# Kernel optimization log

Hardware: AMD Instinct MI355X
Metric: run time of the kernel (lower is better)

Reference implementation:

```python
import jax, jax.numpy as jnp
import numpy as np

B, N, C, D = 16, 2048, 256, 256


def setup_inputs() -> dict:
    key = jax.random.key(0)
    ks = jax.random.split(key, 8)
    x = jax.random.normal(ks[0], (B, N, C), dtype=jnp.float32)
    valid_len = jax.random.randint(ks[1], (B,), 0, N)
    # nn.Linear params: weight [out, in], bias [out]
    s = 1.0 / np.sqrt(C)
    Wq = jax.random.uniform(ks[2], (D, C), dtype=jnp.float32, minval=-s, maxval=s)
    bq = jax.random.uniform(ks[3], (D,), dtype=jnp.float32, minval=-s, maxval=s)
    Wk = jax.random.uniform(ks[4], (D, C), dtype=jnp.float32, minval=-s, maxval=s)
    bk = jax.random.uniform(ks[5], (D,), dtype=jnp.float32, minval=-s, maxval=s)
    Wv = jax.random.uniform(ks[6], (D, C), dtype=jnp.float32, minval=-s, maxval=s)
    bv = jax.random.uniform(ks[7], (D,), dtype=jnp.float32, minval=-s, maxval=s)
    return {"x": x, "valid_len": valid_len, "Wq": Wq, "bq": bq,
            "Wk": Wk, "bk": bk, "Wv": Wv, "bv": bv}


def reference(x, valid_len, Wq, bq, Wk, bk, Wv, bv):
    # QKV projections (nn.Linear: x @ W^T + b)
    q = jnp.einsum('bnc,dc->bnd', x, Wq) + bq
    k = jnp.einsum('bnc,dc->bnd', x, Wk) + bk
    v = jnp.einsum('bnc,dc->bnd', x, Wv) + bv
    # scores [B, N, N] = q @ k^T (no scaling: scale_factor_d unused in forward)
    scores = jnp.einsum('bnd,bmd->bnm', q, k)
    # key-side valid-length mask: arange(N) < valid_len[b], broadcast over queries
    mask = jnp.arange(N)[None, :] < valid_len[:, None]          # [B, N]
    scores = jnp.where(mask[:, None, :], scores, jnp.float32(-1000000.0))
    attn = jax.nn.softmax(scores, axis=-1)
    return jnp.einsum('bnm,bmd->bnd', attn, v)
```

## Files before the change

### kernel.cpp

```cpp
#include <hip/hip_runtime.h>
#include <hip/hip_bf16.h>
#include <stdint.h>

typedef __attribute__((ext_vector_type(8))) _Float16 half8;
typedef __attribute__((ext_vector_type(4))) _Float16 half4;
typedef __attribute__((ext_vector_type(2))) __fp16 fp16x2;
typedef __attribute__((ext_vector_type(4))) float f32x4;
typedef __attribute__((ext_vector_type(16))) float f32x16;
typedef __attribute__((ext_vector_type(4))) float float4v;

#define DEVI static __device__ __forceinline__

constexpr int Bb = 16, Nn = 2048, Cc = 256, Dd = 256;

DEVI unsigned short f2h_bits(float f) {
  _Float16 h = (_Float16)f;
  union { _Float16 h; unsigned short u; } c;
  c.h = h;
  return c.u;
}

DEVI void gl_lds16(const void* gsrc, void* ldst) {
  __builtin_amdgcn_global_load_lds(
      (const __attribute__((address_space(1))) unsigned int*)gsrc,
      (__attribute__((address_space(3))) unsigned int*)ldst, 16, 0, 0);
}

DEVI f32x4 mfma16h(half8 a, half8 b, f32x4 c) {
  return __builtin_amdgcn_mfma_f32_16x16x32_f16(a, b, c, 0, 0, 0);
}
DEVI f32x16 mfma32h(half8 a, half8 b, f32x16 c) {
  return __builtin_amdgcn_mfma_f32_32x32x16_f16(a, b, c, 0, 0, 0);
}

DEVI unsigned int pkrtz(float a, float b) {
  union { fp16x2 h; unsigned int u; } c;
  c.h = __builtin_amdgcn_cvt_pkrtz(a, b);
  return c.u;
}

__global__ void k_split(const float* __restrict__ x, const float* __restrict__ wq,
                        const float* __restrict__ wk, const float* __restrict__ wv,
                        _Float16* __restrict__ xh, _Float16* __restrict__ wh) {
  int i = blockIdx.x * 256 + threadIdx.x;
  if (i < 2097152) {
    float4v v = reinterpret_cast<const float4v*>(x)[i];
    half4 h;
#pragma unroll
    for (int j = 0; j < 4; ++j) h[j] = (_Float16)v[j];
    reinterpret_cast<half4*>(xh)[i] = h;
  } else {
    int ii = i - 2097152;
    int mat = ii >> 16;
    int rem = ii & 65535;
    const float* w = (mat == 0) ? wq : ((mat == 1) ? wk : wv);
    wh[(size_t)mat * 65536 + rem] = (_Float16)w[rem];
  }
}

__global__ __launch_bounds__(256, 2) void k_qkv(
    const _Float16* __restrict__ xh, const _Float16* __restrict__ wh,
    const float* __restrict__ bq, const float* __restrict__ bk, const float* __restrict__ bv,
    _Float16* __restrict__ qout, _Float16* __restrict__ kout, _Float16* __restrict__ vt) {
  __shared__ __align__(16) unsigned short smem[17408];

  const int tid = threadIdx.x;
  const int m0 = blockIdx.x * 128;
  const int n0 = blockIdx.y * 128;
  const int mat = blockIdx.z;
  const _Float16* wmat = wh + (size_t)mat * 65536;
  const int wave = tid >> 6, lane = tid & 63;
  const int wr = wave >> 1, wc = wave & 1;
  const int l15 = lane & 15, lq = lane >> 4;

  f32x4 zero4 = {0.f, 0.f, 0.f, 0.f};
  f32x4 acc[4][4];
#pragma unroll
  for (int a = 0; a < 4; ++a)
#pragma unroll
    for (int b2 = 0; b2 < 4; ++b2) acc[a][b2] = zero4;

  char* As = (char*)smem;
  char* Bs = (char*)smem + 16384;

  for (int kc = 0; kc < 4; ++kc) {
#pragma unroll
    for (int i = 0; i < 4; ++i) {
      int p = i * 4096 + tid * 16;
      int row = p >> 7;
      int src_in_row = (p & 127) ^ ((row & 7) << 4);
      const char* g = (const char*)(xh + (size_t)(m0 + row) * Cc + kc * 64) + src_in_row;
      gl_lds16(g, As + p);
    }
#pragma unroll
    for (int i = 0; i < 4; ++i) {
      int p = i * 4096 + tid * 16;
      int row = p >> 7;
      int src_in_row = (p & 127) ^ ((row & 7) << 4);
      const char* g = (const char*)(wmat + (size_t)(n0 + row) * Cc + kc * 64) + src_in_row;
      gl_lds16(g, Bs + p);
    }
    __syncthreads();
#pragma unroll
    for (int ks = 0; ks < 2; ++ks) {
      half8 af[4], bfr[4];
#pragma unroll
      for (int mf = 0; mf < 4; ++mf) {
        int row = wr * 64 + mf * 16 + l15;
        int byte = (row * 128 + ks * 64 + lq * 16) ^ ((row & 7) << 4);
        af[mf] = *(const half8*)(As + byte);
      }
#pragma unroll
      for (int nf = 0; nf < 4; ++nf) {
        int row = wc * 64 + nf * 16 + l15;
        int byte = (row * 128 + ks * 64 + lq * 16) ^ ((row & 7) << 4);
        bfr[nf] = *(const half8*)(Bs + byte);
      }
#pragma unroll
      for (int mf = 0; mf < 4; ++mf)
#pragma unroll
        for (int nf = 0; nf < 4; ++nf) acc[mf][nf] = mfma16h(af[mf], bfr[nf], acc[mf][nf]);
    }
    __syncthreads();
  }

  const float* bias = (mat == 0) ? bq : ((mat == 1) ? bk : bv);
  if (mat < 2) {
    _Float16* oo = (mat == 0) ? qout : kout;
#pragma unroll
    for (int nf = 0; nf < 4; ++nf) {
      int col = n0 + wc * 64 + nf * 16 + l15;
      float bval = bias[col];
#pragma unroll
      for (int mf = 0; mf < 4; ++mf) {
        int grow = m0 + wr * 64 + mf * 16 + lq * 4;
#pragma unroll
        for (int r = 0; r < 4; ++r)
          oo[(size_t)(grow + r) * Dd + col] = (_Float16)(acc[mf][nf][r] + bval);
      }
    }
  } else {
    __syncthreads();
#pragma unroll
    for (int nf = 0; nf < 4; ++nf) {
      int dl = wc * 64 + nf * 16 + l15;
      float bval = bias[n0 + dl];
#pragma unroll
      for (int mf = 0; mf < 4; ++mf) {
        int nl = wr * 64 + mf * 16 + lq * 4;
#pragma unroll
        for (int r = 0; r < 4; ++r) smem[dl * 136 + nl + r] = f2h_bits(acc[mf][nf][r] + bval);
      }
    }
    __syncthreads();
    const int bbat = m0 >> 11, tok0 = m0 & 2047;
#pragma unroll
    for (int pss = 0; pss < 8; ++pss) {
      int idx = pss * 256 + tid;
      int dl = idx >> 4;
      int cu = idx & 15;
      half8 vval = *(const half8*)((const char*)smem + dl * 272 + cu * 16);
      size_t off = ((size_t)bbat * Dd + n0 + dl) * Nn + tok0 + cu * 8;
      *(half8*)(vt + off) = vval;
    }
  }
}

__global__ __launch_bounds__(256, 2) void k_attn_p(
    const _Float16* __restrict__ qg, const _Float16* __restrict__ kin,
    const _Float16* __restrict__ vt, const int* __restrict__ vlen,
    _Float16* __restrict__ Op, float* __restrict__ ml) {
  __shared__ __align__(16) char SMEM[66048];
  char* const Kb = SMEM;
  char* const Vb = SMEM + 32768;
  unsigned int* const PL = (unsigned int*)SMEM;
  float* const mex = (float*)(SMEM + 65536);

  const int tid = threadIdx.x;
  const int wave = tid >> 6, lane = tid & 63;
  const int l31 = lane & 31, h = lane >> 5;
  const int wq = wave >> 1, wk = wave & 1;
  const int id = blockIdx.x;
  const int g = id & 7;
  const int b = g + 8 * (id >> 9);
  const int q0 = ((id >> 4) & 31) * 64;
  const int kh = (id >> 3) & 1;
  const int kst = kh * 1024;
  const int L = vlen[b];
  const bool uni = (L == 0);
  const int Lk = uni ? Nn : L;
  const int avail = Lk - kst;
  const int nt = (avail > 0) ? ((avail + 63) >> 6 < 16 ? (avail + 63) >> 6 : 16) : 0;
  const size_t prow = (size_t)(b * 2 + kh) * Nn + q0;

  if (nt == 0) {
    if (tid < 64) {
      ml[(prow + tid) * 2 + 0] = -1e30f;
      ml[(prow + tid) * 2 + 1] = 0.f;
    }
    return;
  }

  const char* kbase = (const char*)(kin + (size_t)b * Nn * Dd);
  const char* vbase = (const char*)(vt + (size_t)b * Dd * Nn);
  const char* qbase = (const char*)(qg + ((size_t)b * Nn + q0) * Dd);

#pragma unroll
  for (int i = 0; i < 8; ++i) {
    int p = i * 4096 + tid * 16;
    int row = p >> 9;
    int sl = ((p & 511) >> 4) ^ (row & 31);
    gl_lds16(qbase + (size_t)row * 512 + (sl << 4), Kb + p);
  }
  asm volatile("s_waitcnt vmcnt(0)" ::: "memory");
  asm volatile("s_barrier" ::: "memory");
  half8 qreg[16];
  {
    const int row = wq * 32 + l31;
#pragma unroll
    for (int kt = 0; kt < 16; ++kt) {
      int byte = row * 512 + (((kt * 2 + h) ^ (row & 31)) << 4);
      qreg[kt] = *(const half8*)(Kb + byte);
    }
  }
  asm volatile("s_waitcnt lgkmcnt(0)" ::: "memory");
  asm volatile("s_barrier" ::: "memory");

  f32x16 acc[4];
#pragma unroll
  for (int dg = 0; dg < 4; ++dg)
#pragma unroll
    for (int r = 0; r < 16; ++r) acc[dg][r] = 0.f;
  float m = -__builtin_inff();
  float lsum = 0.f;

  for (int t = 0; t < nt; ++t) {
    const int k0 = kst + t * 64;
#pragma unroll
    for (int i = 0; i < 8; ++i) {
      int p = i * 4096 + tid * 16;
      int row = p >> 9;
      int sl = ((p & 511) >> 4) ^ (row & 31);
      gl_lds16(kbase + (size_t)(k0 + row) * 512 + (sl << 4), Kb + p);
    }
#pragma unroll
    for (int i = 0; i < 8; ++i) {
      int p = i * 4096 + tid * 16;
      int r = p >> 9;
      int sl = ((p & 511) >> 4) ^ (r & 31);
      int cl = sl << 4;
      int d = r * 4 + (cl >> 7);
      int kbyte = cl & 127;
      gl_lds16(vbase + (size_t)d * (Nn * 2) + (size_t)k0 * 2 + kbyte, Vb + p);
    }
    asm volatile("s_waitcnt vmcnt(0)" ::: "memory");
    asm volatile("s_barrier" ::: "memory");

    f32x16 st;
#pragma unroll
    for (int r = 0; r < 16; ++r) st[r] = 0.f;
    if (!uni) {
      const int key = wk * 32 + l31;
      __builtin_amdgcn_s_setprio(1);
#pragma unroll
      for (int kt = 0; kt < 16; ++kt) {
        int byte = key * 512 + (((kt * 2 + h) ^ l31) << 4);
        half8 kf = *(const half8*)(Kb + byte);
        st = mfma32h(kf, qreg[kt], st);
      }
      __builtin_amdgcn_s_setprio(0);
      if (k0 + 64 > L) {
#pragma unroll
        for (int r = 0; r < 16; ++r) {
          int keyg = k0 + wk * 32 + (r & 3) + 8 * (r >> 2) + 4 * h;
          if (keyg >= L) st[r] = -1e6f;
        }
      }
    }

    float pm = st[0];
#pragma unroll
    for (int r = 1; r < 16; ++r) pm = fmaxf(pm, st[r]);
    pm = fmaxf(pm, __shfl_xor(pm, 32));
    if (lane < 32) mex[wave * 32 + lane] = pm;
    asm volatile("s_waitcnt lgkmcnt(0)\ns_barrier" ::: "memory");
    float pmo = mex[(wave ^ 1) * 32 + l31];
    float mnew = fmaxf(m, fmaxf(pm, pmo));
    float scale = __expf(m - mnew);
    m = mnew;
    float psum = 0.f;
#pragma unroll
    for (int r = 0; r < 16; ++r) {
      float p_ = __expf(st[r] - mnew);
      st[r] = p_;
      psum += p_;
    }
    lsum = lsum * scale + psum;

#pragma unroll
    for (int i = 0; i < 8; ++i) {
      unsigned int pk = pkrtz(st[2 * i], st[2 * i + 1]);
      int kp = wk * 16 + 4 * (i >> 1) + (i & 1) + 2 * h;
      PL[wq * 1024 + kp * 32 + l31] = pk;
    }
    asm volatile("s_waitcnt lgkmcnt(0)\ns_barrier" ::: "memory");

    union { unsigned int u[4]; half8 v; } pf0, pf1, pf2, pf3;
#pragma unroll
    for (int w = 0; w < 4; ++w) {
      pf0.u[w] = PL[wq * 1024 + (0 * 8 + h * 4 + w) * 32 + l31];
      pf1.u[w] = PL[wq * 1024 + (1 * 8 + h * 4 + w) * 32 + l31];
      pf2.u[w] = PL[wq * 1024 + (2 * 8 + h * 4 + w) * 32 + l31];
      pf3.u[w] = PL[wq * 1024 + (3 * 8 + h * 4 + w) * 32 + l31];
    }

#pragma unroll
    for (int dg = 0; dg < 4; ++dg)
#pragma unroll
      for (int r = 0; r < 16; ++r) acc[dg][r] *= scale;

    __builtin_amdgcn_s_setprio(1);
#pragma unroll
    for (int dg = 0; dg < 4; ++dg) {
      int r = wk * 32 + dg * 8 + (l31 >> 2);
#pragma unroll
      for (int ks = 0; ks < 4; ++ks) {
        int slot = (l31 & 3) * 8 + ks * 2 + h;
        half8 vf = *(const half8*)(Vb + r * 512 + ((slot ^ (r & 31)) << 4));
        acc[dg] = mfma32h(vf, ks == 0 ? pf0.v : (ks == 1 ? pf1.v : (ks == 2 ? pf2.v : pf3.v)),
                          acc[dg]);
      }
    }
    __builtin_amdgcn_s_setprio(0);

    asm volatile("s_barrier" ::: "memory");
  }

  lsum += __shfl_xor(lsum, 32);
  if (lane < 32) mex[wave * 32 + lane] = lsum;
  asm volatile("s_waitcnt lgkmcnt(0)\ns_barrier" ::: "memory");
  float ltot = lsum + mex[(wave ^ 1) * 32 + l31];
  float linv = 1.f / ltot;

  if (h == 0 && wk == 0) {
    size_t qq = prow + wq * 32 + l31;
    ml[qq * 2 + 0] = m;
    ml[qq * 2 + 1] = ltot;
  }

  _Float16* T = (_Float16*)SMEM;
  {
    const int ql = wq * 32 + l31;
#pragma unroll
    for (int dg = 0; dg < 4; ++dg)
#pragma unroll
      for (int r = 0; r < 16; ++r) {
        int d = wk * 128 + dg * 32 + (r & 3) + 8 * (r >> 2) + 4 * h;
        T[ql * 264 + d] = (_Float16)(acc[dg][r] * linv);
      }
  }
  asm volatile("s_waitcnt lgkmcnt(0)\ns_barrier" ::: "memory");

  {
    const int rb = tid >> 6;
    const int c4 = (tid & 63) * 4;
#pragma unroll
    for (int i = 0; i < 16; ++i) {
      int row = rb + i * 4;
      half4 v = *(const half4*)(T + row * 264 + c4);
      *(half4*)(Op + (prow + row) * Dd + c4) = v;
    }
  }
}

__global__ __launch_bounds__(256) void k_comb(const _Float16* __restrict__ Op,
                                              const float* __restrict__ ml,
                                              float* __restrict__ out) {
  int rid = blockIdx.x * 4 + (threadIdx.x >> 6);
  int lane = threadIdx.x & 63;
  int b = rid >> 11, q = rid & 2047;
  size_t i0 = (size_t)(b * 2 + 0) * Nn + q;
  size_t i1 = (size_t)(b * 2 + 1) * Nn + q;
  float m0 = ml[i0 * 2], l0 = ml[i0 * 2 + 1];
  float m1 = ml[i1 * 2], l1 = ml[i1 * 2 + 1];
  float M = fmaxf(m0, m1);
  float c0 = (l0 > 0.f) ? __expf(m0 - M) * l0 : 0.f;
  float c1 = (l1 > 0.f) ? __expf(m1 - M) * l1 : 0.f;
  float inv = 1.f / (c0 + c1);
  c0 *= inv;
  c1 *= inv;
  float4v o = {0.f, 0.f, 0.f, 0.f};
  {
    half4 o0 = *(const half4*)(Op + i0 * 256 + lane * 4);
#pragma unroll
    for (int j = 0; j < 4; ++j) o[j] = c0 * (float)o0[j];
  }
  if (c1 > 0.f) {
    half4 o1 = *(const half4*)(Op + i1 * 256 + lane * 4);
#pragma unroll
    for (int j = 0; j < 4; ++j) o[j] += c1 * (float)o1[j];
  }
  *(float4v*)(out + ((size_t)b * Nn + q) * 256 + lane * 4) = o;
}

__global__ __launch_bounds__(512, 2) void k_attn(
    const _Float16* __restrict__ qg, const _Float16* __restrict__ kin,
    const _Float16* __restrict__ vt, const int* __restrict__ vlen,
    float* __restrict__ out) {
  __shared__ __align__(16) char SMEM[149504];
  char* const KVb = SMEM;
  unsigned int* const PL = (unsigned int*)(SMEM + 131072);
  float* const mex = (float*)(SMEM + 147456);
  float* const lex = (float*)(SMEM + 148480);

  const int tid = threadIdx.x;
  const int wave = tid >> 6, lane = tid & 63;
  const int l31 = lane & 31, h = lane >> 5;
  const int wq = wave >> 1, wk = wave & 1;
  const int id = blockIdx.x;
  const int g = id & 7;
  const int j = id >> 3;
  const int b = g + 8 * (j >> 4);
  const int q0 = (j & 15) * 128;
  const int L = vlen[b];
  const bool uni = (L == 0);
  const int Lk = uni ? Nn : L;
  const int nt = (Lk + 63) >> 6;

  const char* kbase = (const char*)(kin + (size_t)b * Nn * Dd);
  const char* vbase = (const char*)(vt + (size_t)b * Dd * Nn);
  const char* qbase = (const char*)(qg + ((size_t)b * Nn + q0) * Dd);

  auto STAGE = [&](int buf, int t) {
    char* dst = KVb + buf * 65536;
    const int k0 = t * 64;
#pragma unroll
    for (int i = 0; i < 4; ++i) {
      int p = i * 8192 + tid * 16;
      int row = p >> 9;
      int sl = ((p & 511) >> 4) ^ (row & 31);
      gl_lds16(kbase + (size_t)(k0 + row) * 512 + (sl << 4), dst + p);
    }
#pragma unroll
    for (int i = 0; i < 4; ++i) {
      int p = i * 8192 + tid * 16;
      int r = p >> 9;
      int sl = ((p & 511) >> 4) ^ (r & 31);
      int cl = sl << 4;
      int d = r * 4 + (cl >> 7);
      int kbyte = cl & 127;
      gl_lds16(vbase + (size_t)d * (Nn * 2) + (size_t)k0 * 2 + kbyte, dst + 32768 + p);
    }
  };

  STAGE(0, 0);
#pragma unroll
  for (int i = 0; i < 8; ++i) {
    int p = i * 8192 + tid * 16;
    int row = p >> 9;
    int sl = ((p & 511) >> 4) ^ (row & 31);
    gl_lds16(qbase + (size_t)row * 512 + (sl << 4), KVb + 65536 + p);
  }
  asm volatile("s_waitcnt vmcnt(0)" ::: "memory");
  asm volatile("s_barrier" ::: "memory");

  half8 qreg[16];
  {
    const int row = wq * 32 + l31;
#pragma unroll
    for (int kt = 0; kt < 16; ++kt) {
      int byte = row * 512 + (((kt * 2 + h) ^ (row & 31)) << 4);
      qreg[kt] = *(const half8*)(KVb + 65536 + byte);
    }
  }
  asm volatile("s_waitcnt lgkmcnt(0)" ::: "memory");
  asm volatile("s_barrier" ::: "memory");

  f32x16 acc[4];
#pragma unroll
  for (int dg = 0; dg < 4; ++dg)
#pragma unroll
    for (int r = 0; r < 16; ++r) acc[dg][r] = 0.f;
  float m = -__builtin_inff();
  float lsum = 0.f;

  for (int t = 0; t < nt; ++t) {
    const int cur = t & 1;
    if (t + 1 < nt) {
      STAGE(cur ^ 1, t + 1);
      asm volatile("s_waitcnt vmcnt(8)" ::: "memory");
    } else {
      asm volatile("s_waitcnt vmcnt(0)" ::: "memory");
    }
    asm volatile("s_barrier" ::: "memory");

    const char* Ks = KVb + cur * 65536;
    const char* Vs = Ks + 32768;
    const int k0 = t * 64;

    f32x16 st;
#pragma unroll
    for (int r = 0; r < 16; ++r) st[r] = 0.f;
    if (!uni) {
      const int key = wk * 32 + l31;
      __builtin_amdgcn_s_setprio(1);
#pragma unroll
      for (int kt = 0; kt < 16; ++kt) {
        int byte = key * 512 + (((kt * 2 + h) ^ l31) << 4);
        half8 kf = *(const half8*)(Ks + byte);
        st = mfma32h(kf, qreg[kt], st);
      }
      __builtin_amdgcn_s_setprio(0);
      if (k0 + 64 > L) {
#pragma unroll
        for (int r = 0; r < 16; ++r) {
          int keyg = k0 + wk * 32 + (r & 3) + 8 * (r >> 2) + 4 * h;
          if (keyg >= L) st[r] = -1e6f;
        }
      }
    }

    float pm = st[0];
#pragma unroll
    for (int r = 1; r < 16; ++r) pm = fmaxf(pm, st[r]);
    pm = fmaxf(pm, __shfl_xor(pm, 32));
    if (lane < 32) mex[wave * 32 + lane] = pm;
    asm volatile("s_waitcnt lgkmcnt(0)\ns_barrier" ::: "memory");
    float pmo = mex[(wave ^ 1) * 32 + l31];
    float mnew = fmaxf(m, fmaxf(pm, pmo));
    float scale = __expf(m - mnew);
    m = mnew;
    float psum = 0.f;
#pragma unroll
    for (int r = 0; r < 16; ++r) {
      float p_ = __expf(st[r] - mnew);
      st[r] = p_;
      psum += p_;
    }
    lsum = lsum * scale + psum;

#pragma unroll
    for (int i = 0; i < 8; ++i) {
      unsigned int pk = pkrtz(st[2 * i], st[2 * i + 1]);
      int kp = wk * 16 + 4 * (i >> 1) + (i & 1) + 2 * h;
      PL[wq * 1024 + kp * 32 + l31] = pk;
    }
    asm volatile("s_waitcnt lgkmcnt(0)\ns_barrier" ::: "memory");

    union { unsigned int u[4]; half8 v; } pf0, pf1, pf2, pf3;
#pragma unroll
    for (int w = 0; w < 4; ++w) {
      pf0.u[w] = PL[wq * 1024 + (0 * 8 + h * 4 + w) * 32 + l31];
      pf1.u[w] = PL[wq * 1024 + (1 * 8 + h * 4 + w) * 32 + l31];
      pf2.u[w] = PL[wq * 1024 + (2 * 8 + h * 4 + w) * 32 + l31];
      pf3.u[w] = PL[wq * 1024 + (3 * 8 + h * 4 + w) * 32 + l31];
    }

#pragma unroll
    for (int dg = 0; dg < 4; ++dg)
#pragma unroll
      for (int r = 0; r < 16; ++r) acc[dg][r] *= scale;

    __builtin_amdgcn_s_setprio(1);
#pragma unroll
    for (int dg = 0; dg < 4; ++dg) {
      int r = wk * 32 + dg * 8 + (l31 >> 2);
#pragma unroll
      for (int ks = 0; ks < 4; ++ks) {
        int slot = (l31 & 3) * 8 + ks * 2 + h;
        half8 vf = *(const half8*)(Vs + r * 512 + ((slot ^ (r & 31)) << 4));
        acc[dg] = mfma32h(vf, ks == 0 ? pf0.v : (ks == 1 ? pf1.v : (ks == 2 ? pf2.v : pf3.v)),
                          acc[dg]);
      }
    }
    __builtin_amdgcn_s_setprio(0);

    asm volatile("s_barrier" ::: "memory");
  }

  lsum += __shfl_xor(lsum, 32);
  if (lane < 32) lex[wave * 32 + lane] = lsum;
  asm volatile("s_waitcnt lgkmcnt(0)\ns_barrier" ::: "memory");
  float linv = 1.f / (lsum + lex[(wave ^ 1) * 32 + l31]);

  float* T = (float*)SMEM;
  {
    const int ql = wq * 32 + l31;
#pragma unroll
    for (int dg = 0; dg < 4; ++dg)
#pragma unroll
      for (int r = 0; r < 16; ++r) {
        int d = wk * 128 + dg * 32 + (r & 3) + 8 * (r >> 2) + 4 * h;
        T[ql * 260 + d] = acc[dg][r] * linv;
      }
  }
  asm volatile("s_waitcnt lgkmcnt(0)\ns_barrier" ::: "memory");

  {
    const int rb = tid >> 6;
    const int c4 = (tid & 63) * 4;
#pragma unroll
    for (int i = 0; i < 16; ++i) {
      int row = rb + i * 8;
      float4v v = *(const float4v*)(T + row * 260 + c4);
      *(float4v*)(out + ((size_t)b * Nn + q0 + row) * Dd + c4) = v;
    }
  }
}

extern "C" void kernel_launch(void* const* d_in, const int* in_sizes, int n_in,
                              void* d_out, int out_size, void* d_ws, size_t ws_size,
                              hipStream_t stream) {
  const float* x = (const float*)d_in[0];
  const int* vlen = (const int*)d_in[1];
  const float* Wq = (const float*)d_in[2];
  const float* bq = (const float*)d_in[3];
  const float* Wk = (const float*)d_in[4];
  const float* bk = (const float*)d_in[5];
  const float* Wv = (const float*)d_in[6];
  const float* bv = (const float*)d_in[7];
  float* out = (float*)d_out;
  char* ws = (char*)d_ws;

  _Float16* qh = (_Float16*)(ws);
  _Float16* kk = (_Float16*)(ws + 16777216);
  _Float16* vt = (_Float16*)(ws + 33554432);
  _Float16* wh = (_Float16*)(ws + 50331648);
  _Float16* Op = (_Float16*)(ws + 51380224);
  float* ml = (float*)(ws + 84934656);
  _Float16* xh = (_Float16*)d_out;

  k_split<<<8960, 256, 0, stream>>>(x, Wq, Wk, Wv, xh, wh);
  k_qkv<<<dim3(256, 2, 3), 256, 0, stream>>>(xh, wh, bq, bk, bv, qh, kk, vt);
  if (ws_size >= 85458944ull) {
    k_attn_p<<<1024, 256, 0, stream>>>(qh, kk, vt, vlen, Op, ml);
    k_comb<<<8192, 256, 0, stream>>>(Op, ml, out);
  } else {
    k_attn<<<256, 512, 0, stream>>>(qh, kk, vt, vlen, out);
  }
}
```

Before: 129.5 us.

## Sort attention work items by cost and pair them in persistent double-buffered blocks

A new tiny kernel computes the number of key tiles for each (batch, 128-query tile, key half) item and sorts the items by descending cost. The attention kernel becomes a 256-block, 512-thread persistent kernel in which each block processes the heaviest remaining item paired with the lightest, to even out load across CUs when valid lengths vary. It also double-buffers the K/V tile loads so global-to-LDS copies overlap the MFMA work, and k_comb now skips loading a partial whose weight is zero. The costs are an extra kernel launch, larger LDS use that allows only one block per CU, and a longer dependency chain inside each block.

```diff
diff --git a/kernel.cpp b/kernel.cpp
--- a/kernel.cpp
+++ b/kernel.cpp
@@ -166,210 +166,250 @@
   }
 }
 
-__global__ __launch_bounds__(256, 2) void k_attn_p(
+__global__ void k_order(const int* __restrict__ vlen, int* __restrict__ order) {
+  __shared__ int nts[512];
+  int t = threadIdx.x;
+  int b = t >> 5, kh = t & 1;
+  int L = vlen[b];
+  int Lk = (L == 0) ? Nn : L;
+  int avail = Lk - kh * 1024;
+  int nt = (avail > 0) ? ((avail + 63) >> 6) : 0;
+  nt = nt > 16 ? 16 : nt;
+  nts[t] = nt;
+  __syncthreads();
+  int rank = 0;
+  for (int j = 0; j < 512; ++j) {
+    int nj = nts[j];
+    if (nj > nt || (nj == nt && j < t)) ++rank;
+  }
+  order[rank] = t;
+}
+
+__global__ __launch_bounds__(512, 2) void k_attn_f(
     const _Float16* __restrict__ qg, const _Float16* __restrict__ kin,
     const _Float16* __restrict__ vt, const int* __restrict__ vlen,
-    _Float16* __restrict__ Op, float* __restrict__ ml) {
-  __shared__ __align__(16) char SMEM[66048];
-  char* const Kb = SMEM;
-  char* const Vb = SMEM + 32768;
-  unsigned int* const PL = (unsigned int*)SMEM;
-  float* const mex = (float*)(SMEM + 65536);
+    const int* __restrict__ order, _Float16* __restrict__ Op,
+    float* __restrict__ ml) {
+  __shared__ __align__(16) char SMEM[149504];
+  char* const KVb = SMEM;
+  unsigned int* const PL = (unsigned int*)(SMEM + 131072);
+  float* const mex = (float*)(SMEM + 147456);
+  float* const lex = (float*)(SMEM + 148480);
 
   const int tid = threadIdx.x;
   const int wave = tid >> 6, lane = tid & 63;
   const int l31 = lane & 31, h = lane >> 5;
   const int wq = wave >> 1, wk = wave & 1;
-  const int id = blockIdx.x;
-  const int g = id & 7;
-  const int b = g + 8 * (id >> 9);
-  const int q0 = ((id >> 4) & 31) * 64;
-  const int kh = (id >> 3) & 1;
-  const int kst = kh * 1024;
-  const int L = vlen[b];
-  const bool uni = (L == 0);
-  const int Lk = uni ? Nn : L;
-  const int avail = Lk - kst;
-  const int nt = (avail > 0) ? ((avail + 63) >> 6 < 16 ? (avail + 63) >> 6 : 16) : 0;
-  const size_t prow = (size_t)(b * 2 + kh) * Nn + q0;
-
-  if (nt == 0) {
-    if (tid < 64) {
-      ml[(prow + tid) * 2 + 0] = -1e30f;
-      ml[(prow + tid) * 2 + 1] = 0.f;
-    }
-    return;
-  }
-
-  const char* kbase = (const char*)(kin + (size_t)b * Nn * Dd);
-  const char* vbase = (const char*)(vt + (size_t)b * Dd * Nn);
-  const char* qbase = (const char*)(qg + ((size_t)b * Nn + q0) * Dd);
-
-#pragma unroll
-  for (int i = 0; i < 8; ++i) {
-    int p = i * 4096 + tid * 16;
-    int row = p >> 9;
-    int sl = ((p & 511) >> 4) ^ (row & 31);
-    gl_lds16(qbase + (size_t)row * 512 + (sl << 4), Kb + p);
-  }
-  asm volatile("s_waitcnt vmcnt(0)" ::: "memory");
-  asm volatile("s_barrier" ::: "memory");
-  half8 qreg[16];
-  {
-    const int row = wq * 32 + l31;
-#pragma unroll
-    for (int kt = 0; kt < 16; ++kt) {
-      int byte = row * 512 + (((kt * 2 + h) ^ (row & 31)) << 4);
-      qreg[kt] = *(const half8*)(Kb + byte);
-    }
-  }
-  asm volatile("s_waitcnt lgkmcnt(0)" ::: "memory");
-  asm volatile("s_barrier" ::: "memory");
-
-  f32x16 acc[4];
-#pragma unroll
-  for (int dg = 0; dg < 4; ++dg)
-#pragma unroll
-    for (int r = 0; r < 16; ++r) acc[dg][r] = 0.f;
-  float m = -__builtin_inff();
-  float lsum = 0.f;
-
-  for (int t = 0; t < nt; ++t) {
-    const int k0 = kst + t * 64;
+
+  for (int s = 0; s < 2; ++s) {
+    const int item = order[s == 0 ? blockIdx.x : (511 - blockIdx.x)];
+    const int b = item >> 5;
+    const int q0 = ((item >> 1) & 15) * 128;
+    const int kh = item & 1;
+    const int kst = kh * 1024;
+    const int L = vlen[b];
+    const bool uni = (L == 0);
+    const int Lk = uni ? Nn : L;
+    const int avail = Lk - kst;
+    int nt = (avail > 0) ? ((avail + 63) >> 6) : 0;
+    nt = nt > 16 ? 16 : nt;
+    const size_t prow = (size_t)(b * 2 + kh) * Nn + q0;
+
+    if (nt == 0) {
+      if (tid < 128) {
+        ml[(prow + tid) * 2 + 0] = -1e30f;
+        ml[(prow + tid) * 2 + 1] = 0.f;
+      }
+      continue;
+    }
+
+    const char* kbase = (const char*)(kin + (size_t)b * Nn * Dd);
+    const char* vbase = (const char*)(vt + (size_t)b * Dd * Nn);
+    const char* qbase = (const char*)(qg + ((size_t)b * Nn + q0) * Dd);
+
+    auto STAGE = [&](int buf, int t) {
+      char* dst = KVb + buf * 65536;
+      const int k0 = kst + t * 64;
+#pragma unroll
+      for (int i = 0; i < 4; ++i) {
+        int p = i * 8192 + tid * 16;
+        int row = p >> 9;
+        int sl = ((p & 511) >> 4) ^ (row & 31);
+        gl_lds16(kbase + (size_t)(k0 + row) * 512 + (sl << 4), dst + p);
+      }
+#pragma unroll
+      for (int i = 0; i < 4; ++i) {
+        int p = i * 8192 + tid * 16;
+        int r = p >> 9;
+        int sl = ((p & 511) >> 4) ^ (r & 31);
+        int cl = sl << 4;
+        int d = r * 4 + (cl >> 7);
+        int kbyte = cl & 127;
+        gl_lds16(vbase + (size_t)d * (Nn * 2) + (size_t)k0 * 2 + kbyte, dst + 32768 + p);
+      }
+    };
+
+    STAGE(0, 0);
 #pragma unroll
     for (int i = 0; i < 8; ++i) {
-      int p = i * 4096 + tid * 16;
+      int p = i * 8192 + tid * 16;
       int row = p >> 9;
       int sl = ((p & 511) >> 4) ^ (row & 31);
-      gl_lds16(kbase + (size_t)(k0 + row) * 512 + (sl << 4), Kb + p);
-    }
-#pragma unroll
-    for (int i = 0; i < 8; ++i) {
-      int p = i * 4096 + tid * 16;
-      int r = p >> 9;
-      int sl = ((p & 511) >> 4) ^ (r & 31);
-      int cl = sl << 4;
-      int d = r * 4 + (cl >> 7);
-      int kbyte = cl & 127;
-      gl_lds16(vbase + (size_t)d * (Nn * 2) + (size_t)k0 * 2 + kbyte, Vb + p);
+      gl_lds16(qbase + (size_t)row * 512 + (sl << 4), KVb + 65536 + p);
     }
     asm volatile("s_waitcnt vmcnt(0)" ::: "memory");
     asm volatile("s_barrier" ::: "memory");
 
-    f32x16 st;
-#pragma unroll
-    for (int r = 0; r < 16; ++r) st[r] = 0.f;
-    if (!uni) {
-      const int key = wk * 32 + l31;
+    half8 qreg[16];
+    {
+      const int row = wq * 32 + l31;
+#pragma unroll
+      for (int kt = 0; kt < 16; ++kt) {
+        int byte = row * 512 + (((kt * 2 + h) ^ (row & 31)) << 4);
+        qreg[kt] = *(const half8*)(KVb + 65536 + byte);
+      }
+    }
+    asm volatile("s_waitcnt lgkmcnt(0)" ::: "memory");
+    asm volatile("s_barrier" ::: "memory");
+
+    f32x16 acc[4];
+#pragma unroll
+    for (int dg = 0; dg < 4; ++dg)
+#pragma unroll
+      for (int r = 0; r < 16; ++r) acc[dg][r] = 0.f;
+    float m = -__builtin_inff();
+    float lsum = 0.f;
+
+    for (int t = 0; t < nt; ++t) {
+      const int cur = t & 1;
+      if (t + 1 < nt) {
+        STAGE(cur ^ 1, t + 1);
+        asm volatile("s_waitcnt vmcnt(8)" ::: "memory");
+      } else {
+        asm volatile("s_waitcnt vmcnt(0)" ::: "memory");
+      }
+      asm volatile("s_barrier" ::: "memory");
+
+      const char* Ks = KVb + cur * 65536;
+      const char* Vs = Ks + 32768;
+      const int k0 = kst + t * 64;
+
+      f32x16 st;
+#pragma unroll
+      for (int r = 0; r < 16; ++r) st[r] = 0.f;
+      if (!uni) {
+        const int key = wk * 32 + l31;
+        __builtin_amdgcn_s_setprio(1);
+#pragma unroll
+        for (int kt = 0; kt < 16; ++kt) {
+          int byte = key * 512 + (((kt * 2 + h) ^ l31) << 4);
+          half8 kf = *(const half8*)(Ks + byte);
+          st = mfma32h(kf, qreg[kt], st);
+        }
+        __builtin_amdgcn_s_setprio(0);
+        if (k0 + 64 > L) {
+#pragma unroll
+          for (int r = 0; r < 16; ++r) {
+            int keyg = k0 + wk * 32 + (r & 3) + 8 * (r >> 2) + 4 * h;
+            if (keyg >= L) st[r] = -1e6f;
+          }
+        }
+      }
+
+      float pm = st[0];
+#pragma unroll
+      for (int r = 1; r < 16; ++r) pm = fmaxf(pm, st[r]);
+      pm = fmaxf(pm, __shfl_xor(pm, 32));
+      if (lane < 32) mex[wave * 32 + lane] = pm;
+      asm volatile("s_waitcnt lgkmcnt(0)\ns_barrier" ::: "memory");
+      float pmo = mex[(wave ^ 1) * 32 + l31];
+      float mnew = fmaxf(m, fmaxf(pm, pmo));
+      float scale = __expf(m - mnew);
+      m = mnew;
+      float psum = 0.f;
+#pragma unroll
+      for (int r = 0; r < 16; ++r) {
+        float p_ = __expf(st[r] - mnew);
+        st[r] = p_;
+        psum += p_;
+      }
+      lsum = lsum * scale + psum;
+
+#pragma unroll
+      for (int i = 0; i < 8; ++i) {
+        unsigned int pk = pkrtz(st[2 * i], st[2 * i + 1]);
+        int kp = wk * 16 + 4 * (i >> 1) + (i & 1) + 2 * h;
+        PL[wq * 1024 + kp * 32 + l31] = pk;
+      }
+      asm volatile("s_waitcnt lgkmcnt(0)\ns_barrier" ::: "memory");
+
+      union { unsigned int u[4]; half8 v; } pf0, pf1, pf2, pf3;
+#pragma unroll
+      for (int w = 0; w < 4; ++w) {
+        pf0.u[w] = PL[wq * 1024 + (0 * 8 + h * 4 + w) * 32 + l31];
+        pf1.u[w] = PL[wq * 1024 + (1 * 8 + h * 4 + w) * 32 + l31];
+        pf2.u[w] = PL[wq * 1024 + (2 * 8 + h * 4 + w) * 32 + l31];
+        pf3.u[w] = PL[wq * 1024 + (3 * 8 + h * 4 + w) * 32 + l31];
+      }
+
+#pragma unroll
+      for (int dg = 0; dg < 4; ++dg)
+#pragma unroll
+        for (int r = 0; r < 16; ++r) acc[dg][r] *= scale;
+
       __builtin_amdgcn_s_setprio(1);
 #pragma unroll
-      for (int kt = 0; kt < 16; ++kt) {
-        int byte = key * 512 + (((kt * 2 + h) ^ l31) << 4);
-        half8 kf = *(const half8*)(Kb + byte);
-        st = mfma32h(kf, qreg[kt], st);
+      for (int dg = 0; dg < 4; ++dg) {
+        int r = wk * 32 + dg * 8 + (l31 >> 2);
+#pragma unroll
+        for (int ks = 0; ks < 4; ++ks) {
+          int slot = (l31 & 3) * 8 + ks * 2 + h;
+          half8 vf = *(const half8*)(Vs + r * 512 + ((slot ^ (r & 31)) << 4));
+          acc[dg] = mfma32h(vf, ks == 0 ? pf0.v : (ks == 1 ? pf1.v : (ks == 2 ? pf2.v : pf3.v)),
+                            acc[dg]);
+        }
       }
       __builtin_amdgcn_s_setprio(0);
-      if (k0 + 64 > L) {
+
+      asm volatile("s_barrier" ::: "memory");
+    }
+
+    lsum += __shfl_xor(lsum, 32);
+    if (lane < 32) lex[wave * 32 + lane] = lsum;
+    asm volatile("s_waitcnt lgkmcnt(0)\ns_barrier" ::: "memory");
+    float ltot = lsum + lex[(wave ^ 1) * 32 + l31];
+    float linv = 1.f / ltot;
+
+    if (h == 0 && wk == 0) {
+      size_t qq = prow + wq * 32 + l31;
+      ml[qq * 2 + 0] = m;
+      ml[qq * 2 + 1] = ltot;
+    }
+
+    _Float16* T = (_Float16*)SMEM;
+    {
+      const int ql = wq * 32 + l31;
+#pragma unroll
+      for (int dg = 0; dg < 4; ++dg)
 #pragma unroll
         for (int r = 0; r < 16; ++r) {
-          int keyg = k0 + wk * 32 + (r & 3) + 8 * (r >> 2) + 4 * h;
-          if (keyg >= L) st[r] = -1e6f;
+          int d = wk * 128 + dg * 32 + (r & 3) + 8 * (r >> 2) + 4 * h;
+          T[ql * 264 + d] = (_Float16)(acc[dg][r] * linv);
         }
-      }
-    }
-
-    float pm = st[0];
-#pragma unroll
-    for (int r = 1; r < 16; ++r) pm = fmaxf(pm, st[r]);
-    pm = fmaxf(pm, __shfl_xor(pm, 32));
-    if (lane < 32) mex[wave * 32 + lane] = pm;
+    }
     asm volatile("s_waitcnt lgkmcnt(0)\ns_barrier" ::: "memory");
-    float pmo = mex[(wave ^ 1) * 32 + l31];
-    float mnew = fmaxf(m, fmaxf(pm, pmo));
-    float scale = __expf(m - mnew);
-    m = mnew;
-    float psum = 0.f;
-#pragma unroll
-    for (int r = 0; r < 16; ++r) {
-      float p_ = __expf(st[r] - mnew);
-      st[r] = p_;
-      psum += p_;
-    }
-    lsum = lsum * scale + psum;
-
-#pragma unroll
-    for (int i = 0; i < 8; ++i) {
-      unsigned int pk = pkrtz(st[2 * i], st[2 * i + 1]);
-      int kp = wk * 16 + 4 * (i >> 1) + (i & 1) + 2 * h;
-      PL[wq * 1024 + kp * 32 + l31] = pk;
+
+    {
+      const int rb = tid >> 6;
+      const int c4 = (tid & 63) * 4;
+#pragma unroll
+      for (int i = 0; i < 16; ++i) {
+        int row = rb + i * 8;
+        half4 v = *(const half4*)(T + row * 264 + c4);
+        *(half4*)(Op + (prow + row) * Dd + c4) = v;
+      }
     }
     asm volatile("s_waitcnt lgkmcnt(0)\ns_barrier" ::: "memory");
-
-    union { unsigned int u[4]; half8 v; } pf0, pf1, pf2, pf3;
-#pragma unroll
-    for (int w = 0; w < 4; ++w) {
-      pf0.u[w] = PL[wq * 1024 + (0 * 8 + h * 4 + w) * 32 + l31];
-      pf1.u[w] = PL[wq * 1024 + (1 * 8 + h * 4 + w) * 32 + l31];
-      pf2.u[w] = PL[wq * 1024 + (2 * 8 + h * 4 + w) * 32 + l31];
-      pf3.u[w] = PL[wq * 1024 + (3 * 8 + h * 4 + w) * 32 + l31];
-    }
-
-#pragma unroll
-    for (int dg = 0; dg < 4; ++dg)
-#pragma unroll
-      for (int r = 0; r < 16; ++r) acc[dg][r] *= scale;
-
-    __builtin_amdgcn_s_setprio(1);
-#pragma unroll
-    for (int dg = 0; dg < 4; ++dg) {
-      int r = wk * 32 + dg * 8 + (l31 >> 2);
-#pragma unroll
-      for (int ks = 0; ks < 4; ++ks) {
-        int slot = (l31 & 3) * 8 + ks * 2 + h;
-        half8 vf = *(const half8*)(Vb + r * 512 + ((slot ^ (r & 31)) << 4));
-        acc[dg] = mfma32h(vf, ks == 0 ? pf0.v : (ks == 1 ? pf1.v : (ks == 2 ? pf2.v : pf3.v)),
-                          acc[dg]);
-      }
-    }
-    __builtin_amdgcn_s_setprio(0);
-
-    asm volatile("s_barrier" ::: "memory");
-  }
-
-  lsum += __shfl_xor(lsum, 32);
-  if (lane < 32) mex[wave * 32 + lane] = lsum;
-  asm volatile("s_waitcnt lgkmcnt(0)\ns_barrier" ::: "memory");
-  float ltot = lsum + mex[(wave ^ 1) * 32 + l31];
-  float linv = 1.f / ltot;
-
-  if (h == 0 && wk == 0) {
-    size_t qq = prow + wq * 32 + l31;
-    ml[qq * 2 + 0] = m;
-    ml[qq * 2 + 1] = ltot;
-  }
-
-  _Float16* T = (_Float16*)SMEM;
-  {
-    const int ql = wq * 32 + l31;
-#pragma unroll
-    for (int dg = 0; dg < 4; ++dg)
-#pragma unroll
-      for (int r = 0; r < 16; ++r) {
-        int d = wk * 128 + dg * 32 + (r & 3) + 8 * (r >> 2) + 4 * h;
-        T[ql * 264 + d] = (_Float16)(acc[dg][r] * linv);
-      }
-  }
-  asm volatile("s_waitcnt lgkmcnt(0)\ns_barrier" ::: "memory");
-
-  {
-    const int rb = tid >> 6;
-    const int c4 = (tid & 63) * 4;
-#pragma unroll
-    for (int i = 0; i < 16; ++i) {
-      int row = rb + i * 4;
-      half4 v = *(const half4*)(T + row * 264 + c4);
-      *(half4*)(Op + (prow + row) * Dd + c4) = v;
-    }
   }
 }
 
@@ -390,7 +430,7 @@
   c0 *= inv;
   c1 *= inv;
   float4v o = {0.f, 0.f, 0.f, 0.f};
-  {
+  if (c0 > 0.f) {
     half4 o0 = *(const half4*)(Op + i0 * 256 + lane * 4);
 #pragma unroll
     for (int j = 0; j < 4; ++j) o[j] = c0 * (float)o0[j];
@@ -628,12 +668,14 @@
   _Float16* wh = (_Float16*)(ws + 50331648);
   _Float16* Op = (_Float16*)(ws + 51380224);
   float* ml = (float*)(ws + 84934656);
+  int* order = (int*)(ws + 85458944);
   _Float16* xh = (_Float16*)d_out;
 
   k_split<<<8960, 256, 0, stream>>>(x, Wq, Wk, Wv, xh, wh);
   k_qkv<<<dim3(256, 2, 3), 256, 0, stream>>>(xh, wh, bq, bk, bv, qh, kk, vt);
-  if (ws_size >= 85458944ull) {
-    k_attn_p<<<1024, 256, 0, stream>>>(qh, kk, vt, vlen, Op, ml);
+  if (ws_size >= 85460992ull) {
+    k_order<<<1, 512, 0, stream>>>(vlen, order);
+    k_attn_f<<<256, 512, 0, stream>>>(qh, kk, vt, vlen, order, Op, ml);
     k_comb<<<8192, 256, 0, stream>>>(Op, ml, out);
   } else {
     k_attn<<<256, 512, 0, stream>>>(qh, kk, vt, vlen, out);
```

After: 140.1 us. +8.2%, slower.
